# Kernel tuning notes

Measured on AMD Instinct MI355X. Metric: run time of the kernel, lower is better.

The kernel has to match this reference:

```python
import jax, jax.numpy as jnp
import numpy as np

S = 8          # nodes per subgraph (last node is the anchor)
B = 8192       # number of subgraphs in the batch
N = B * S      # total nodes
E_PER = S * S  # edges per subgraph (dense local connectivity)
DIN, DOUT = 512, 256
EPS = 1e-12


def _block_edges(key):
    # local src/dst in [0,S) per subgraph, offset to global node ids
    k1, k2 = jax.random.split(key)
    src = jax.random.randint(k1, (B, E_PER), 0, S)
    dst = jax.random.randint(k2, (B, E_PER), 0, S)
    off = (jnp.arange(B) * S)[:, None]
    return (src + off).reshape(-1), (dst + off).reshape(-1)


def setup_inputs() -> dict:
    key = jax.random.key(0)
    ks = jax.random.split(key, 10)
    pos_src, pos_dst = _block_edges(ks[0])
    neg_src, neg_dst = _block_edges(ks[1])
    return {
        "pos_x": jax.random.normal(ks[2], (N, DIN), jnp.float32),
        "neg_x": jax.random.normal(ks[3], (N, DIN), jnp.float32),
        "pos_src": pos_src, "pos_dst": pos_dst,
        "pos_w": jax.random.uniform(ks[4], (B * E_PER,), jnp.float32),
        "neg_src": neg_src, "neg_dst": neg_dst,
        "neg_w": jax.random.uniform(ks[5], (B * E_PER,), jnp.float32),
        "W_gcn": jax.random.normal(ks[6], (DIN, DOUT), jnp.float32) / np.sqrt(DIN),
        "b_gcn": jnp.zeros((DOUT,), jnp.float32),
        "prelu_a": jnp.float32(0.25),
        "W_bil": jax.random.normal(ks[7], (DOUT, DOUT), jnp.float32) / np.sqrt(DOUT),
        "b_bil": jnp.zeros((1,), jnp.float32),
    }


def _l2norm(x):
    return x / jnp.maximum(jnp.linalg.norm(x, axis=1, keepdims=True), EPS)


def _gcn_branch(x, src, dst, w, W_gcn, b_gcn, prelu_a):
    # GraphConv(norm='none') with edge weights: h = A_w (X W) + b
    xw = x @ W_gcn                                      # [N, DOUT]
    agg = jnp.zeros_like(xw).at[dst].add(w[:, None] * xw[src])
    h = agg + b_gcn
    h = jnp.where(h >= 0, h, prelu_a * h)               # PReLU (single param)
    h = h.reshape(B, S, -1)                             # fixed-size subgraphs
    pool = jnp.mean(h[:, :-1], axis=1)                  # mean over non-anchor nodes
    anchor = h[:, -1]                                   # last node per subgraph
    return _l2norm(pool), _l2norm(anchor)


def reference(pos_x, neg_x, pos_src, pos_dst, pos_w, neg_src, neg_dst, neg_w,
              W_gcn, b_gcn, prelu_a, W_bil, b_bil):
    pos_pool, anchor = _gcn_branch(pos_x, pos_src, pos_dst, pos_w, W_gcn, b_gcn, prelu_a)
    neg_pool, _ = _gcn_branch(neg_x, neg_src, neg_dst, neg_w, W_gcn, b_gcn, prelu_a)
    # Bilinear(D, D, 1): score_b = pool_b^T W anchor_b + bias
    pos_scores = jnp.einsum('bd,de,be->b', pos_pool, W_bil, anchor) + b_bil[0]
    neg_scores = jnp.einsum('bd,de,be->b', neg_pool, W_bil, anchor) + b_bil[0]
    return pos_scores, neg_scores
```

## Files before the change

kernel.cpp:

```cpp
#include <hip/hip_runtime.h>
#include <stdint.h>
#include <math.h>

#define SS 8
#define NBLK 8192
#define DIN 512
#define DOUT 256
#define GB 8
#define MT 64
#define BK 32
#define KSTEPS 16
#define VSTR 264
#define EPSN 1e-12f

typedef __bf16 bf16;
typedef __bf16 bf16x8 __attribute__((ext_vector_type(8)));
typedef float  f32x4  __attribute__((ext_vector_type(4)));

typedef __attribute__((address_space(3))) uint32_t       lds_u32;
typedef __attribute__((address_space(1))) const uint32_t g_u32;

__device__ __forceinline__ void dma16(const void* g, void* l) {
    __builtin_amdgcn_global_load_lds((g_u32*)g, (lds_u32*)l, 16, 0, 0);
}

__device__ __forceinline__ bf16x8 cvt8(f32x4 lo, f32x4 hi) {
    bf16x8 r;
    r[0] = (bf16)lo[0]; r[1] = (bf16)lo[1]; r[2] = (bf16)lo[2]; r[3] = (bf16)lo[3];
    r[4] = (bf16)hi[0]; r[5] = (bf16)hi[1]; r[6] = (bf16)hi[2]; r[7] = (bf16)hi[3];
    return r;
}

__global__ void prep_kernel(const float* __restrict__ W_gcn,
                            const float* __restrict__ W_bil,
                            bf16* __restrict__ Wt,
                            bf16* __restrict__ Wh,
                            bf16* __restrict__ Wl) {
    int idx = blockIdx.x * 256 + threadIdx.x;
    if (idx < DIN * DOUT) {
        int k = idx >> 8, n = idx & 255;
        Wt[((size_t)(k >> 5) * DOUT + n) * BK + (k & 31)] = (bf16)W_gcn[idx];
    } else {
        int j = idx - DIN * DOUT;
        float wv = W_bil[j];
        bf16 h = (bf16)wv;
        Wh[j] = h;
        Wl[j] = (bf16)(wv - (float)h);
    }
}

__global__ __launch_bounds__(512, 4) void cola_fused7(
    const float* __restrict__ pos_x, const float* __restrict__ neg_x,
    const int* __restrict__ pos_src, const int* __restrict__ pos_dst,
    const float* __restrict__ pos_w,
    const int* __restrict__ neg_src, const int* __restrict__ neg_dst,
    const float* __restrict__ neg_w,
    const bf16* __restrict__ Wt, const bf16* __restrict__ Wh,
    const bf16* __restrict__ Wl,
    const float* __restrict__ b_gcn, const float* __restrict__ prelu_a,
    const float* __restrict__ b_bil, float* __restrict__ out)
{
    __shared__ __align__(16) float bufA[3][2][MT * BK];
    __shared__ float adjP[GB][SS][SS];
    __shared__ float adjN[GB][SS][SS];
    __shared__ float red[5 * GB];

    float* pool_pos = (float*)&bufA[0][0][0];
    float* v_lds    = pool_pos + GB * DOUT;
    bf16*  ahs      = (bf16*)&bufA[1][0][0];
    bf16*  als      = ahs + GB * VSTR;

    const int t    = threadIdx.x;
    const int wg   = blockIdx.x;
    const int w    = t >> 6;
    const int b    = w >> 2;
    const int wq   = w & 3;
    const int lane = t & 63;
    const int q    = lane >> 4;
    const int r15  = lane & 15;
    const int row0 = wg * MT;

    for (int i = t; i < GB * 64; i += 512) { ((float*)adjP)[i] = 0.f; ((float*)adjN)[i] = 0.f; }
    if (t < 5 * GB) red[t] = 0.f;
    __syncthreads();

    {
        int   sp = pos_src[wg * 512 + t];
        int   dp = pos_dst[wg * 512 + t];
        float wp = pos_w[wg * 512 + t];
        int   sn = neg_src[wg * 512 + t];
        int   dn = neg_dst[wg * 512 + t];
        float wn = neg_w[wg * 512 + t];
        int gl = t >> 6;
        int base = (wg * GB + gl) * SS;
        atomicAdd(&adjP[gl][dp - base][sp - base], wp);
        atomicAdd(&adjN[gl][dn - base][sn - base], wn);
    }

    const int arow_off = lane >> 3;
    const int akq      = (lane & 7) ^ arow_off;
    const float* xb    = (b == 0) ? pos_x : neg_x;

    auto issueA = [&](int s, int bufi) {
        const int kbase = s * BK;
#pragma unroll
        for (int h = 0; h < 2; ++h) {
            int c = wq * 2 + h;
            int row = c * 8 + arow_off;
            dma16(xb + (size_t)(row0 + row) * DIN + kbase + akq * 4,
                  &bufA[bufi][b][c * 256]);
        }
    };

    auto loadB = [&](bf16x8* dst, int s) {
#pragma unroll
        for (int ni = 0; ni < 4; ++ni)
            dst[ni] = *(const bf16x8*)(Wt +
                ((size_t)s * DOUT + wq * 64 + ni * 16 + r15) * BK + q * 8);
    };

    f32x4 acc[4][4];
#pragma unroll
    for (int mi = 0; mi < 4; ++mi)
#pragma unroll
        for (int ni = 0; ni < 4; ++ni)
            acc[mi][ni] = (f32x4){0.f, 0.f, 0.f, 0.f};

    bf16x8 breg[2][4];

    issueA(0, 0);
    loadB(breg[0], 0);
    issueA(1, 1);

#pragma unroll
    for (int s = 0; s < KSTEPS; ++s) {
        if (s == KSTEPS - 1)
            asm volatile("s_waitcnt vmcnt(0) lgkmcnt(0)" ::: "memory");
        else
            asm volatile("s_waitcnt vmcnt(2) lgkmcnt(0)" ::: "memory");
        __builtin_amdgcn_s_barrier();
        __builtin_amdgcn_sched_barrier(0);

        if (s + 1 < KSTEPS) loadB(breg[(s + 1) & 1], s + 1);
        if (s + 2 < KSTEPS) issueA(s + 2, (s + 2) % 3);

        const int bufi = s % 3;
        const bf16x8* bfv = breg[s & 1];
        const int q0 = (2 * q) ^ (r15 & 7);
        const int q1 = q0 ^ 1;
        bf16x8 af[4];
#pragma unroll
        for (int mi = 0; mi < 4; ++mi) {
            int m = mi * 16 + r15;
            f32x4 lo = *(const f32x4*)&bufA[bufi][b][m * BK + q0 * 4];
            f32x4 hi = *(const f32x4*)&bufA[bufi][b][m * BK + q1 * 4];
            af[mi] = cvt8(lo, hi);
        }
#pragma unroll
        for (int mi = 0; mi < 4; ++mi)
#pragma unroll
            for (int ni = 0; ni < 4; ++ni)
                acc[mi][ni] = __builtin_amdgcn_mfma_f32_16x16x32_bf16(
                    af[mi], bfv[ni], acc[mi][ni], 0, 0, 0);
    }
    __syncthreads();

    const float pa = *prelu_a;

    if (w < 4) {
#pragma unroll
        for (int mi = 0; mi < 4; ++mi) {
            const int gl = mi * 2 + (q >> 1);
            float part = 0.f;
#pragma unroll
            for (int ni = 0; ni < 4; ++ni) {
                float r0, r1, r2, r3, r4, r5, r6, r7;
#pragma unroll
                for (int r = 0; r < 4; ++r) {
                    float own = acc[mi][ni][r];
                    float oth = __shfl_xor(own, 16);
                    float lo = ((q & 1) == 0) ? own : oth;
                    float hi = ((q & 1) == 0) ? oth : own;
                    if (r == 0) { r0 = lo; r4 = hi; }
                    else if (r == 1) { r1 = lo; r5 = hi; }
                    else if (r == 2) { r2 = lo; r6 = hi; }
                    else            { r3 = lo; r7 = hi; }
                }
                int c = wq * 64 + ni * 16 + r15;
                float bg = b_gcn[c];
                float pool = 0.f, anch = 0.f;
#pragma unroll
                for (int d = 0; d < 8; ++d) {
                    const float* ar = &adjP[gl][d][0];
                    float a = bg + ar[0]*r0 + ar[1]*r1 + ar[2]*r2 + ar[3]*r3
                                 + ar[4]*r4 + ar[5]*r5 + ar[6]*r6 + ar[7]*r7;
                    float h = (a >= 0.f) ? a : pa * a;
                    if (d < 7) pool += h; else anch = h;
                }
                float pl = pool * (1.f / 7.f);
                if ((q & 1) == 0) {
                    pool_pos[gl * DOUT + c] = pl;
                    part += pl * pl;
                } else {
                    bf16 hh = (bf16)anch;
                    ahs[gl * VSTR + c] = hh;
                    als[gl * VSTR + c] = (bf16)(anch - (float)hh);
                    part += anch * anch;
                }
            }
            part += __shfl_xor(part, 8);
            part += __shfl_xor(part, 4);
            part += __shfl_xor(part, 2);
            part += __shfl_xor(part, 1);
            if (r15 == 0) atomicAdd((q & 1) ? &red[GB + gl] : &red[gl], part);
        }
    }
    __syncthreads();

    {
        f32x4 accv[2];
        accv[0] = (f32x4){0.f, 0.f, 0.f, 0.f};
        accv[1] = (f32x4){0.f, 0.f, 0.f, 0.f};
        const int ga = (r15 & 7) * VSTR;
#pragma unroll
        for (int ks = 0; ks < 8; ++ks) {
            bf16x8 ah_f = *(const bf16x8*)(ahs + ga + ks * 32 + q * 8);
            bf16x8 al_f = *(const bf16x8*)(als + ga + ks * 32 + q * 8);
#pragma unroll
            for (int ni = 0; ni < 2; ++ni) {
                int d = w * 32 + ni * 16 + r15;
                bf16x8 bh = *(const bf16x8*)(Wh + (size_t)d * DOUT + ks * 32 + q * 8);
                bf16x8 bl = *(const bf16x8*)(Wl + (size_t)d * DOUT + ks * 32 + q * 8);
                accv[ni] = __builtin_amdgcn_mfma_f32_16x16x32_bf16(ah_f, bh, accv[ni], 0, 0, 0);
                accv[ni] = __builtin_amdgcn_mfma_f32_16x16x32_bf16(al_f, bh, accv[ni], 0, 0, 0);
                accv[ni] = __builtin_amdgcn_mfma_f32_16x16x32_bf16(ah_f, bl, accv[ni], 0, 0, 0);
            }
        }
        float sp[4] = {0.f, 0.f, 0.f, 0.f};
        if (q < 2) {
#pragma unroll
            for (int ni = 0; ni < 2; ++ni) {
                int c = w * 32 + ni * 16 + r15;
#pragma unroll
                for (int r = 0; r < 4; ++r) {
                    int g = q * 4 + r;
                    v_lds[g * DOUT + c] = accv[ni][r];
                    sp[r] += accv[ni][r] * pool_pos[g * DOUT + c];
                }
            }
        }
#pragma unroll
        for (int r = 0; r < 4; ++r) {
            sp[r] += __shfl_xor(sp[r], 8);
            sp[r] += __shfl_xor(sp[r], 4);
            sp[r] += __shfl_xor(sp[r], 2);
            sp[r] += __shfl_xor(sp[r], 1);
        }
        if (q < 2 && r15 == 0) {
#pragma unroll
            for (int r = 0; r < 4; ++r) atomicAdd(&red[3 * GB + q * 4 + r], sp[r]);
        }
    }
    __syncthreads();

    if (w >= 4) {
#pragma unroll
        for (int mi = 0; mi < 4; ++mi) {
            const int gl = mi * 2 + (q >> 1);
            float part = 0.f;
#pragma unroll
            for (int ni = 0; ni < 4; ++ni) {
                float r0, r1, r2, r3, r4, r5, r6, r7;
#pragma unroll
                for (int r = 0; r < 4; ++r) {
                    float own = acc[mi][ni][r];
                    float oth = __shfl_xor(own, 16);
                    float lo = ((q & 1) == 0) ? own : oth;
                    float hi = ((q & 1) == 0) ? oth : own;
                    if (r == 0) { r0 = lo; r4 = hi; }
                    else if (r == 1) { r1 = lo; r5 = hi; }
                    else if (r == 2) { r2 = lo; r6 = hi; }
                    else            { r3 = lo; r7 = hi; }
                }
                int c = wq * 64 + ni * 16 + r15;
                float bg = b_gcn[c];
                float pool = 0.f;
#pragma unroll
                for (int d = 0; d < 7; ++d) {
                    const float* ar = &adjN[gl][d][0];
                    float a = bg + ar[0]*r0 + ar[1]*r1 + ar[2]*r2 + ar[3]*r3
                                 + ar[4]*r4 + ar[5]*r5 + ar[6]*r6 + ar[7]*r7;
                    float h = (a >= 0.f) ? a : pa * a;
                    pool += h;
                }
                float pl = pool * (1.f / 7.f);
                part += ((q & 1) == 0) ? pl * v_lds[gl * DOUT + c] : pl * pl;
            }
            part += __shfl_xor(part, 8);
            part += __shfl_xor(part, 4);
            part += __shfl_xor(part, 2);
            part += __shfl_xor(part, 1);
            if (r15 == 0) atomicAdd((q & 1) ? &red[2 * GB + gl] : &red[4 * GB + gl], part);
        }
    }
    __syncthreads();

    if (t < GB) {
        float np = fmaxf(sqrtf(red[t]), EPSN);
        float na = fmaxf(sqrtf(red[GB + t]), EPSN);
        float nn = fmaxf(sqrtf(red[2 * GB + t]), EPSN);
        float bb = b_bil[0];
        out[wg * GB + t]        = red[3 * GB + t] / (np * na) + bb;
        out[NBLK + wg * GB + t] = red[4 * GB + t] / (nn * na) + bb;
    }
}

extern "C" void kernel_launch(void* const* d_in, const int* in_sizes, int n_in,
                              void* d_out, int out_size, void* d_ws, size_t ws_size,
                              hipStream_t stream) {
    const float* pos_x   = (const float*)d_in[0];
    const float* neg_x   = (const float*)d_in[1];
    const int*   pos_src = (const int*)d_in[2];
    const int*   pos_dst = (const int*)d_in[3];
    const float* pos_w   = (const float*)d_in[4];
    const int*   neg_src = (const int*)d_in[5];
    const int*   neg_dst = (const int*)d_in[6];
    const float* neg_w   = (const float*)d_in[7];
    const float* W_gcn   = (const float*)d_in[8];
    const float* b_gcn   = (const float*)d_in[9];
    const float* prelu_a = (const float*)d_in[10];
    const float* W_bil   = (const float*)d_in[11];
    const float* b_bil   = (const float*)d_in[12];
    float* outp = (float*)d_out;

    bf16* Wt = (bf16*)d_ws;
    bf16* Wh = Wt + DIN * DOUT;
    bf16* Wl = Wh + DOUT * DOUT;

    prep_kernel<<<(DIN * DOUT + DOUT * DOUT) / 256, 256, 0, stream>>>(W_gcn, W_bil, Wt, Wh, Wl);
    cola_fused7<<<NBLK / GB, 512, 0, stream>>>(
        pos_x, neg_x, pos_src, pos_dst, pos_w, neg_src, neg_dst, neg_w,
        Wt, Wh, Wl, b_gcn, prelu_a, b_bil, outp);
}
```

Baseline: 396.6 us.

## Halve row tile and stage W_gcn through LDS via async DMA image

Halves the per-workgroup tile to 4 subgraphs (32 rows), which doubles the grid and halves the accumulator registers. The GCN weight is repacked in the prep kernel into a fragment-ordered image. Each k-step now DMAs that image into double-buffered LDS instead of every wave loading its B fragments from global into registers. The aim is more resident workgroups and latency hiding, and sharing B loads across waves. In exchange, W_gcn is streamed twice as many times overall, LDS usage per block grows, and the bilinear stage uses only a quarter of its MFMA rows.

```diff
diff --git a/kernel.cpp b/kernel.cpp
--- a/kernel.cpp
+++ b/kernel.cpp
@@ -6,8 +6,8 @@
 #define NBLK 8192
 #define DIN 512
 #define DOUT 256
-#define GB 8
-#define MT 64
+#define GB 4
+#define MT 32
 #define BK 32
 #define KSTEPS 16
 #define VSTR 264
@@ -33,13 +33,21 @@
 
 __global__ void prep_kernel(const float* __restrict__ W_gcn,
                             const float* __restrict__ W_bil,
-                            bf16* __restrict__ Wt,
+                            bf16* __restrict__ WtImg,
                             bf16* __restrict__ Wh,
                             bf16* __restrict__ Wl) {
     int idx = blockIdx.x * 256 + threadIdx.x;
     if (idx < DIN * DOUT) {
         int k = idx >> 8, n = idx & 255;
-        Wt[((size_t)(k >> 5) * DOUT + n) * BK + (k & 31)] = (bf16)W_gcn[idx];
+        int s  = k >> 5;
+        int qq = (k >> 3) & 3;
+        int j  = k & 7;
+        int wq = n >> 6;
+        int ni = (n >> 4) & 3;
+        int r  = n & 15;
+        int l  = qq * 16 + r;
+        size_t pos = ((size_t)(((s * 4 + wq) * 4 + ni) * 64) + l) * 8 + j;
+        WtImg[pos] = (bf16)W_gcn[idx];
     } else {
         int j = idx - DIN * DOUT;
         float wv = W_bil[j];
@@ -49,18 +57,19 @@
     }
 }
 
-__global__ __launch_bounds__(512, 4) void cola_fused7(
+__global__ __launch_bounds__(512, 4) void cola_fused8(
     const float* __restrict__ pos_x, const float* __restrict__ neg_x,
     const int* __restrict__ pos_src, const int* __restrict__ pos_dst,
     const float* __restrict__ pos_w,
     const int* __restrict__ neg_src, const int* __restrict__ neg_dst,
     const float* __restrict__ neg_w,
-    const bf16* __restrict__ Wt, const bf16* __restrict__ Wh,
+    const bf16* __restrict__ WtImg, const bf16* __restrict__ Wh,
     const bf16* __restrict__ Wl,
     const float* __restrict__ b_gcn, const float* __restrict__ prelu_a,
     const float* __restrict__ b_bil, float* __restrict__ out)
 {
     __shared__ __align__(16) float bufA[3][2][MT * BK];
+    __shared__ __align__(16) bf16  bufB[2][16 * 512];
     __shared__ float adjP[GB][SS][SS];
     __shared__ float adjN[GB][SS][SS];
     __shared__ float red[5 * GB];
@@ -80,21 +89,23 @@
     const int r15  = lane & 15;
     const int row0 = wg * MT;
 
-    for (int i = t; i < GB * 64; i += 512) { ((float*)adjP)[i] = 0.f; ((float*)adjN)[i] = 0.f; }
+    if (t < GB * 64) { ((float*)adjP)[t] = 0.f; ((float*)adjN)[t] = 0.f; }
     if (t < 5 * GB) red[t] = 0.f;
     __syncthreads();
 
     {
-        int   sp = pos_src[wg * 512 + t];
-        int   dp = pos_dst[wg * 512 + t];
-        float wp = pos_w[wg * 512 + t];
-        int   sn = neg_src[wg * 512 + t];
-        int   dn = neg_dst[wg * 512 + t];
-        float wn = neg_w[wg * 512 + t];
-        int gl = t >> 6;
+        int e  = t & 255;
+        int br = t >> 8;
+        const int*   srcA = br ? neg_src : pos_src;
+        const int*   dstA = br ? neg_dst : pos_dst;
+        const float* wA   = br ? neg_w   : pos_w;
+        float* adj = br ? &adjN[0][0][0] : &adjP[0][0][0];
+        int   sv = srcA[wg * 256 + e];
+        int   dv = dstA[wg * 256 + e];
+        float wv = wA[wg * 256 + e];
+        int gl = e >> 6;
         int base = (wg * GB + gl) * SS;
-        atomicAdd(&adjP[gl][dp - base][sp - base], wp);
-        atomicAdd(&adjN[gl][dn - base][sn - base], wn);
+        atomicAdd(&adj[gl * 64 + (dv - base) * SS + (sv - base)], wv);
     }
 
     const int arow_off = lane >> 3;
@@ -102,34 +113,28 @@
     const float* xb    = (b == 0) ? pos_x : neg_x;
 
     auto issueA = [&](int s, int bufi) {
-        const int kbase = s * BK;
+        int row = wq * 8 + arow_off;
+        dma16(xb + (size_t)(row0 + row) * DIN + s * BK + akq * 4,
+              &bufA[bufi][b][wq * 256]);
+    };
+    auto issueB = [&](int s, int bufi) {
 #pragma unroll
         for (int h = 0; h < 2; ++h) {
-            int c = wq * 2 + h;
-            int row = c * 8 + arow_off;
-            dma16(xb + (size_t)(row0 + row) * DIN + kbase + akq * 4,
-                  &bufA[bufi][b][c * 256]);
+            int c = w * 2 + h;
+            dma16(WtImg + ((size_t)s * 16 + c) * 512 + lane * 8,
+                  &bufB[bufi][c * 512]);
         }
     };
 
-    auto loadB = [&](bf16x8* dst, int s) {
-#pragma unroll
-        for (int ni = 0; ni < 4; ++ni)
-            dst[ni] = *(const bf16x8*)(Wt +
-                ((size_t)s * DOUT + wq * 64 + ni * 16 + r15) * BK + q * 8);
-    };
-
-    f32x4 acc[4][4];
-#pragma unroll
-    for (int mi = 0; mi < 4; ++mi)
+    f32x4 acc[2][4];
+#pragma unroll
+    for (int mi = 0; mi < 2; ++mi)
 #pragma unroll
         for (int ni = 0; ni < 4; ++ni)
             acc[mi][ni] = (f32x4){0.f, 0.f, 0.f, 0.f};
 
-    bf16x8 breg[2][4];
-
     issueA(0, 0);
-    loadB(breg[0], 0);
+    issueB(0, 0);
     issueA(1, 1);
 
 #pragma unroll
@@ -137,27 +142,32 @@
         if (s == KSTEPS - 1)
             asm volatile("s_waitcnt vmcnt(0) lgkmcnt(0)" ::: "memory");
         else
-            asm volatile("s_waitcnt vmcnt(2) lgkmcnt(0)" ::: "memory");
+            asm volatile("s_waitcnt vmcnt(1) lgkmcnt(0)" ::: "memory");
         __builtin_amdgcn_s_barrier();
         __builtin_amdgcn_sched_barrier(0);
 
-        if (s + 1 < KSTEPS) loadB(breg[(s + 1) & 1], s + 1);
+        if (s + 1 < KSTEPS) issueB(s + 1, (s + 1) & 1);
         if (s + 2 < KSTEPS) issueA(s + 2, (s + 2) % 3);
 
         const int bufi = s % 3;
-        const bf16x8* bfv = breg[s & 1];
+        const int bcur = s & 1;
+        bf16x8 bfv[4];
+#pragma unroll
+        for (int ni = 0; ni < 4; ++ni)
+            bfv[ni] = *(const bf16x8*)&bufB[bcur][(wq * 4 + ni) * 512 + lane * 8];
+
         const int q0 = (2 * q) ^ (r15 & 7);
         const int q1 = q0 ^ 1;
-        bf16x8 af[4];
-#pragma unroll
-        for (int mi = 0; mi < 4; ++mi) {
+        bf16x8 af[2];
+#pragma unroll
+        for (int mi = 0; mi < 2; ++mi) {
             int m = mi * 16 + r15;
             f32x4 lo = *(const f32x4*)&bufA[bufi][b][m * BK + q0 * 4];
             f32x4 hi = *(const f32x4*)&bufA[bufi][b][m * BK + q1 * 4];
             af[mi] = cvt8(lo, hi);
         }
 #pragma unroll
-        for (int mi = 0; mi < 4; ++mi)
+        for (int mi = 0; mi < 2; ++mi)
 #pragma unroll
             for (int ni = 0; ni < 4; ++ni)
                 acc[mi][ni] = __builtin_amdgcn_mfma_f32_16x16x32_bf16(
@@ -169,7 +179,7 @@
 
     if (w < 4) {
 #pragma unroll
-        for (int mi = 0; mi < 4; ++mi) {
+        for (int mi = 0; mi < 2; ++mi) {
             const int gl = mi * 2 + (q >> 1);
             float part = 0.f;
 #pragma unroll
@@ -221,7 +231,7 @@
         f32x4 accv[2];
         accv[0] = (f32x4){0.f, 0.f, 0.f, 0.f};
         accv[1] = (f32x4){0.f, 0.f, 0.f, 0.f};
-        const int ga = (r15 & 7) * VSTR;
+        const int ga = (r15 & 3) * VSTR;
 #pragma unroll
         for (int ks = 0; ks < 8; ++ks) {
             bf16x8 ah_f = *(const bf16x8*)(ahs + ga + ks * 32 + q * 8);
@@ -237,15 +247,14 @@
             }
         }
         float sp[4] = {0.f, 0.f, 0.f, 0.f};
-        if (q < 2) {
+        if (q == 0) {
 #pragma unroll
             for (int ni = 0; ni < 2; ++ni) {
-                int c = w * 32 + ni * 16 + r15;
+                int d = w * 32 + ni * 16 + r15;
 #pragma unroll
                 for (int r = 0; r < 4; ++r) {
-                    int g = q * 4 + r;
-                    v_lds[g * DOUT + c] = accv[ni][r];
-                    sp[r] += accv[ni][r] * pool_pos[g * DOUT + c];
+                    v_lds[r * DOUT + d] = accv[ni][r];
+                    sp[r] += accv[ni][r] * pool_pos[r * DOUT + d];
                 }
             }
         }
@@ -256,16 +265,16 @@
             sp[r] += __shfl_xor(sp[r], 2);
             sp[r] += __shfl_xor(sp[r], 1);
         }
-        if (q < 2 && r15 == 0) {
-#pragma unroll
-            for (int r = 0; r < 4; ++r) atomicAdd(&red[3 * GB + q * 4 + r], sp[r]);
+        if (q == 0 && r15 == 0) {
+#pragma unroll
+            for (int r = 0; r < 4; ++r) atomicAdd(&red[3 * GB + r], sp[r]);
         }
     }
     __syncthreads();
 
     if (w >= 4) {
 #pragma unroll
-        for (int mi = 0; mi < 4; ++mi) {
+        for (int mi = 0; mi < 2; ++mi) {
             const int gl = mi * 2 + (q >> 1);
             float part = 0.f;
 #pragma unroll
@@ -333,12 +342,12 @@
     const float* b_bil   = (const float*)d_in[12];
     float* outp = (float*)d_out;
 
-    bf16* Wt = (bf16*)d_ws;
-    bf16* Wh = Wt + DIN * DOUT;
-    bf16* Wl = Wh + DOUT * DOUT;
-
-    prep_kernel<<<(DIN * DOUT + DOUT * DOUT) / 256, 256, 0, stream>>>(W_gcn, W_bil, Wt, Wh, Wl);
-    cola_fused7<<<NBLK / GB, 512, 0, stream>>>(
+    bf16* WtImg = (bf16*)d_ws;
+    bf16* Wh    = WtImg + DIN * DOUT;
+    bf16* Wl    = Wh + DOUT * DOUT;
+
+    prep_kernel<<<(DIN * DOUT + DOUT * DOUT) / 256, 256, 0, stream>>>(W_gcn, W_bil, WtImg, Wh, Wl);
+    cola_fused8<<<NBLK / GB, 512, 0, stream>>>(
         pos_x, neg_x, pos_src, pos_dst, pos_w, neg_src, neg_dst, neg_w,
-        Wt, Wh, Wl, b_gcn, prelu_a, b_bil, outp);
-}
+        WtImg, Wh, Wl, b_gcn, prelu_a, b_bil, outp);
+}
```

Measured after the change: 389.2 us. About the same (-1.9%).
